# Optimization experiments

Hardware: AMD Instinct MI355X
Metric: run time of the kernel (lower is better)

## Reference

```python
import jax, jax.numpy as jnp
import numpy as np

MAX_FRAMES = 12
EMBED_DIM = 512
TOPK = 12
NUM_SAMPLES = 500
SIGMA = 0.05
SEL_DIM = 2
NUM_HEADS = 2


def setup_inputs() -> dict:
    key = jax.random.key(0)
    ks = jax.random.split(key, 9)
    D = EMBED_DIM
    C = D // 2
    s = lambda fan_in: 1.0 / np.sqrt(fan_in)
    return {
        "x": jax.random.normal(ks[0], (16, MAX_FRAMES * 50, D), dtype=jnp.float32),
        "ln_g": jnp.ones((D,), jnp.float32),
        "ln_b": jnp.zeros((D,), jnp.float32),
        "w_in": jax.random.normal(ks[1], (D, C), jnp.float32) * s(D),
        "wq": jax.random.normal(ks[2], (C, C), jnp.float32) * s(C),
        "wk": jax.random.normal(ks[3], (C, C), jnp.float32) * s(C),
        "wv": jax.random.normal(ks[4], (C, C), jnp.float32) * s(C),
        "wo": jax.random.normal(ks[5], (C, C), jnp.float32) * s(C),
        "w1": jax.random.normal(ks[6], (2 * C, C), jnp.float32) * s(2 * C),
        "w2": jax.random.normal(ks[7], (C, 1), jnp.float32) * s(C),
    }


def layer_norm(x, g, b, eps=1e-5):
    mu = jnp.mean(x, axis=-1, keepdims=True)
    var = jnp.var(x, axis=-1, keepdims=True)
    return (x - mu) * jax.lax.rsqrt(var + eps) * g + b


def mha(x, wq, wk, wv, wo):
    B, N, C = x.shape
    hd = C // NUM_HEADS
    q = (x @ wq).reshape(B, N, NUM_HEADS, hd).transpose(0, 2, 1, 3)
    k = (x @ wk).reshape(B, N, NUM_HEADS, hd).transpose(0, 2, 1, 3)
    v = (x @ wv).reshape(B, N, NUM_HEADS, hd).transpose(0, 2, 1, 3)
    attn = jax.nn.softmax(jnp.einsum('bhnd,bhmd->bhnm', q, k) / np.sqrt(hd), axis=-1)
    out = jnp.einsum('bhnm,bhmd->bhnd', attn, v).transpose(0, 2, 1, 3).reshape(B, N, C)
    return out @ wo


def predictor(x, ln_g, ln_b, w_in, wq, wk, wv, wo, w1, w2):
    h = jax.nn.gelu(layer_norm(x, ln_g, ln_b) @ w_in, approximate=False)
    h = mha(h, wq, wk, wv, wo)
    B, N, C = h.shape
    g = jnp.mean(h, axis=1, keepdims=True)
    h = jnp.concatenate([h, jnp.broadcast_to(g, (B, N, C))], axis=-1)
    h = jax.nn.gelu(h @ w1, approximate=False)
    return jnp.tanh(h @ w2)  # (B, N, 1)


def perturbed_topk(scores):
    # scores: (b, d) -> soft indicators (b, k, d)
    b, d = scores.shape
    noise = jax.random.normal(jax.random.key(1), (b, NUM_SAMPLES, d), dtype=scores.dtype)
    perturbed = scores[:, None, :] + noise * SIGMA
    _, idx = jax.lax.top_k(perturbed, TOPK)            # (b, ns, k)
    idx = jnp.sort(idx, axis=-1)
    onehot = jax.nn.one_hot(idx, d, dtype=scores.dtype)  # (b, ns, k, d)
    return onehot.mean(axis=1)                          # (b, k, d)


def reference(x, ln_g, ln_b, w_in, wq, wk, wv, wo, w1, w2):
    B, L, D = x.shape
    N = L // MAX_FRAMES
    xf = x.reshape(B * MAX_FRAMES, N, D)
    pred = predictor(xf, ln_g, ln_b, w_in, wq, wk, wv, wo, w1, w2)[..., 0]  # (b, N)
    spatial_score = pred[:, SEL_DIM:]                    # (b, N-2)
    ind = perturbed_topk(spatial_score)                  # (b, k, N-2)
    cls_feat = xf[:, :SEL_DIM, :]
    spatial_feat = xf[:, SEL_DIM:, :]
    sel = jnp.einsum('bkl,bld->bkd', ind, spatial_feat)
    out = jnp.concatenate([cls_feat, sel], axis=1)       # (b, 2+k, D)
    return out.reshape(B, -1, D)
```

## Files before the change

### kernel.cpp

```cpp
#include <hip/hip_runtime.h>
#include <stdint.h>

#define B2      192
#define NTOK    50
#define ROWS    9600
#define D_EMB   512
#define C_DIM   256
#define HD      128
#define NSAMP   500
#define TOPKK   12
#define NSPA    48
#define NSAMP_T 96000
#define NOISE_OFF 61953536ull
#define NOISE_BYTES 18432000ull
#define WS_NEED (NOISE_OFF + NOISE_BYTES)

typedef short short8 __attribute__((ext_vector_type(8)));
typedef float f32x4  __attribute__((ext_vector_type(4)));

__device__ __forceinline__ float gelu_f(float x) {
    return 0.5f * x * (1.0f + erff(x * 0.7071067811865476f));
}
__device__ __forceinline__ uint16_t f2bf(float x) {
    uint32_t u = __float_as_uint(x);
    return (uint16_t)((u + 0x7fffu + ((u >> 16) & 1u)) >> 16);
}
__device__ __forceinline__ float bf2f(uint16_t b) {
    return __uint_as_float(((uint32_t)b) << 16);
}
__device__ __forceinline__ size_t swzA(int m, int k, int K) {
    return ((size_t)(m >> 4) * (K >> 5) + (k >> 5)) * 512
         + (size_t)((((k >> 3) & 3) * 16 + (m & 15)) * 8 + (k & 7));
}

__device__ __forceinline__ uint32_t rotl32(uint32_t x, int r) {
    return (x << r) | (x >> (32 - r));
}
__device__ __forceinline__ void threefry01(uint32_t& x0, uint32_t& x1) {
    const uint32_t ks0 = 0u, ks1 = 1u, ks2 = 0x1BD11BDBu;
    x0 += ks0; x1 += ks1;
#define TFR(r) { x0 += x1; x1 = rotl32(x1, r); x1 ^= x0; }
    TFR(13) TFR(15) TFR(26) TFR(6)  x0 += ks1; x1 += ks2 + 1u;
    TFR(17) TFR(29) TFR(16) TFR(24) x0 += ks2; x1 += ks0 + 2u;
    TFR(13) TFR(15) TFR(26) TFR(6)  x0 += ks0; x1 += ks1 + 3u;
    TFR(17) TFR(29) TFR(16) TFR(24) x0 += ks1; x1 += ks2 + 4u;
    TFR(13) TFR(15) TFR(26) TFR(6)  x0 += ks2; x1 += ks0 + 5u;
#undef TFR
}

__device__ __forceinline__ float erfinv_xla(float x) {
    float w = -log1pf(-x * x);
    float p;
    if (w < 5.0f) {
        w -= 2.5f;
        p = 2.81022636e-08f;
        p = fmaf(p, w, 3.43273939e-07f);
        p = fmaf(p, w, -3.5233877e-06f);
        p = fmaf(p, w, -4.39150654e-06f);
        p = fmaf(p, w, 0.00021858087f);
        p = fmaf(p, w, -0.00125372503f);
        p = fmaf(p, w, -0.00417768164f);
        p = fmaf(p, w, 0.246640727f);
        p = fmaf(p, w, 1.50140941f);
    } else {
        w = sqrtf(w) - 3.0f;
        p = -0.000200214257f;
        p = fmaf(p, w, 0.000100950558f);
        p = fmaf(p, w, 0.00134934322f);
        p = fmaf(p, w, -0.00367342844f);
        p = fmaf(p, w, 0.00573950773f);
        p = fmaf(p, w, -0.0076224613f);
        p = fmaf(p, w, 0.00943887047f);
        p = fmaf(p, w, 1.00167406f);
        p = fmaf(p, w, 2.83297682f);
    }
    return p * x;
}

__device__ __forceinline__ float bits_to_normal(uint32_t bits) {
    float f = __uint_as_float((bits >> 9) | 0x3f800000u) - 1.0f;
    float u = f * 2.0f + (-0.99999994039535522461f);
    u = fmaxf(-0.99999994039535522461f, u);
    return 1.4142135623730951f * erfinv_xla(u);
}

__global__ __launch_bounds__(256) void noise_kernel(float* __restrict__ noise) {
    int T  = blockIdx.x * 256 + threadIdx.x;
    int q  = T / NSAMP_T;
    int g2 = T - q * NSAMP_T;
    uint32_t cbase = (uint32_t)g2 * 48u + (uint32_t)(q * 4);
    float4 o;
    { uint32_t x0=0u, x1=cbase + 0u; threefry01(x0,x1); o.x = bits_to_normal(x0^x1) * 0.05f; }
    { uint32_t x0=0u, x1=cbase + 1u; threefry01(x0,x1); o.y = bits_to_normal(x0^x1) * 0.05f; }
    { uint32_t x0=0u, x1=cbase + 2u; threefry01(x0,x1); o.z = bits_to_normal(x0^x1) * 0.05f; }
    { uint32_t x0=0u, x1=cbase + 3u; threefry01(x0,x1); o.w = bits_to_normal(x0^x1) * 0.05f; }
    ((float4*)noise)[(size_t)q * NSAMP_T + g2] = o;
}

__global__ __launch_bounds__(256) void prep_kernel(const float* __restrict__ x,
                                                   const float* __restrict__ g,
                                                   const float* __restrict__ b,
                                                   short* __restrict__ xh,
                                                   short* __restrict__ xl,
                                                   const float* __restrict__ w_in, const float* __restrict__ wq,
                                                   const float* __restrict__ wk, const float* __restrict__ wv,
                                                   const float* __restrict__ wo, const float* __restrict__ w1,
                                                   short* win_hi, short* win_lo, short* wq_hi, short* wq_lo,
                                                   short* wk_hi, short* wk_lo, short* wv_hi, short* wv_lo,
                                                   short* wo_hi, short* wo_lo, short* w1a_hi, short* w1a_lo) {
    if (blockIdx.x < 2400) {
        int row  = blockIdx.x * 4 + (threadIdx.x >> 6);
        int lane = threadIdx.x & 63;
        const float* rp = x + (size_t)row * D_EMB;
        float4 v0 = *(const float4*)(rp + lane * 8);
        float4 v1 = *(const float4*)(rp + lane * 8 + 4);
        float s  = v0.x + v0.y + v0.z + v0.w + v1.x + v1.y + v1.z + v1.w;
        float s2 = v0.x*v0.x + v0.y*v0.y + v0.z*v0.z + v0.w*v0.w
                 + v1.x*v1.x + v1.y*v1.y + v1.z*v1.z + v1.w*v1.w;
#pragma unroll
        for (int off = 32; off; off >>= 1) {
            s  += __shfl_xor(s,  off);
            s2 += __shfl_xor(s2, off);
        }
        float mu  = s / 512.0f;
        float var = s2 / 512.0f - mu * mu;
        float inv = 1.0f / sqrtf(var + 1e-5f);
        const float* gp = g + lane * 8;
        const float* bp = b + lane * 8;
        float o[8];
        o[0]=(v0.x-mu)*inv*gp[0]+bp[0]; o[1]=(v0.y-mu)*inv*gp[1]+bp[1];
        o[2]=(v0.z-mu)*inv*gp[2]+bp[2]; o[3]=(v0.w-mu)*inv*gp[3]+bp[3];
        o[4]=(v1.x-mu)*inv*gp[4]+bp[4]; o[5]=(v1.y-mu)*inv*gp[5]+bp[5];
        o[6]=(v1.z-mu)*inv*gp[6]+bp[6]; o[7]=(v1.w-mu)*inv*gp[7]+bp[7];
        short8 h8, l8;
#pragma unroll
        for (int j = 0; j < 8; ++j) {
            uint16_t h = f2bf(o[j]);
            h8[j] = (short)h;
            l8[j] = (short)f2bf(o[j] - bf2f(h));
        }
        size_t blk = (size_t)(row >> 4) * 16 + (lane >> 2);
        int inner  = (lane & 3) * 16 + (row & 15);
        ((short8*)xh)[blk * 64 + inner] = h8;
        ((short8*)xl)[blk * 64 + inner] = l8;
    } else {
        int blk = blockIdx.x - 2400;
        const float* W; short *hi, *lo; int K, base;
        if      (blk <  64) { W = w_in; hi = win_hi; lo = win_lo; K = 512; base = 0;   }
        else if (blk <  96) { W = wq;   hi = wq_hi;  lo = wq_lo;  K = 256; base = 64;  }
        else if (blk < 128) { W = wk;   hi = wk_hi;  lo = wk_lo;  K = 256; base = 96;  }
        else if (blk < 160) { W = wv;   hi = wv_hi;  lo = wv_lo;  K = 256; base = 128; }
        else if (blk < 192) { W = wo;   hi = wo_hi;  lo = wo_lo;  K = 256; base = 160; }
        else                { W = w1;   hi = w1a_hi; lo = w1a_lo; K = 256; base = 192; }
        int t = (blk - base) * 256 + threadIdx.x;
        int n = t & 255, k8 = t >> 8;
        short8 h8, l8;
#pragma unroll
        for (int j = 0; j < 8; ++j) {
            float wvl = W[(size_t)(k8 * 8 + j) * 256 + n];
            uint16_t h = f2bf(wvl);
            h8[j] = (short)h;
            l8[j] = (short)f2bf(wvl - bf2f(h));
        }
        size_t bb = (size_t)(n >> 4) * (K >> 5) + (k8 >> 2);
        int inner = (k8 & 3) * 16 + (n & 15);
        ((short8*)hi)[bb * 64 + inner] = h8;
        ((short8*)lo)[bb * 64 + inner] = l8;
    }
}

template<int KB>
__device__ __forceinline__ void mm_core(const short8* __restrict__ pAh, const short8* __restrict__ pAl,
                                        const short8* __restrict__ pBh0, const short8* __restrict__ pBl0,
                                        const short8* __restrict__ pBh1, const short8* __restrict__ pBl1,
                                        f32x4& acc0, f32x4& acc1) {
    short8 ah[3], al[3], bh0[3], bl0[3], bh1[3], bl1[3];
#pragma unroll
    for (int i = 0; i < 2; ++i) {
        int off = i * 64;
        ah[i] = pAh[off];  al[i] = pAl[off];
        bh0[i] = pBh0[off]; bl0[i] = pBl0[off];
        bh1[i] = pBh1[off]; bl1[i] = pBl1[off];
    }
#pragma unroll
    for (int ks = 0; ks < KB; ++ks) {
        int cur = ks % 3;
        if (ks + 2 < KB) {
            int pre = (ks + 2) % 3, off = (ks + 2) * 64;
            ah[pre] = pAh[off];  al[pre] = pAl[off];
            bh0[pre] = pBh0[off]; bl0[pre] = pBl0[off];
            bh1[pre] = pBh1[off]; bl1[pre] = pBl1[off];
        }
        acc0 = __builtin_amdgcn_mfma_f32_16x16x32_bf16(ah[cur], bh0[cur], acc0, 0, 0, 0);
        acc0 = __builtin_amdgcn_mfma_f32_16x16x32_bf16(ah[cur], bl0[cur], acc0, 0, 0, 0);
        acc0 = __builtin_amdgcn_mfma_f32_16x16x32_bf16(al[cur], bh0[cur], acc0, 0, 0, 0);
        acc1 = __builtin_amdgcn_mfma_f32_16x16x32_bf16(ah[cur], bh1[cur], acc1, 0, 0, 0);
        acc1 = __builtin_amdgcn_mfma_f32_16x16x32_bf16(ah[cur], bl1[cur], acc1, 0, 0, 0);
        acc1 = __builtin_amdgcn_mfma_f32_16x16x32_bf16(al[cur], bh1[cur], acc1, 0, 0, 0);
    }
}

__device__ __forceinline__ void epi_store(f32x4 acc, int row0, int col, int N,
                                          float* __restrict__ Cf, short* __restrict__ Chi,
                                          short* __restrict__ Clo,
                                          const float* __restrict__ bias, int act) {
#pragma unroll
    for (int r = 0; r < 4; ++r) {
        int row = row0 + r;
        float v2 = acc[r];
        if (bias) v2 += bias[(size_t)(row / 50) * N + col];
        if (act)  v2 = gelu_f(v2);
        if (Cf) Cf[(size_t)row * N + col] = v2;
        if (Chi) {
            uint16_t h = f2bf(v2);
            size_t ad = swzA(row, col, 256);
            Chi[ad] = (short)h;
            Clo[ad] = (short)f2bf(v2 - bf2f(h));
        }
    }
}

template<int KB>
__global__ __launch_bounds__(256) void gemm_one(const short8* __restrict__ Ah,
                                                const short8* __restrict__ Al,
                                                const short8* __restrict__ Bh,
                                                const short8* __restrict__ Bl,
                                                float* __restrict__ Cf,
                                                short* __restrict__ Chi,
                                                short* __restrict__ Clo,
                                                const float* __restrict__ bias,
                                                int act) {
    int lane = threadIdx.x & 63;
    int wv   = threadIdx.x >> 6;
    int ms   = blockIdx.x * 4 + wv;
    int ns0  = blockIdx.y * 2;
    const short8* pAh  = Ah + (size_t)ms  * KB * 64 + lane;
    const short8* pAl  = Al + (size_t)ms  * KB * 64 + lane;
    const short8* pBh0 = Bh + (size_t)ns0 * KB * 64 + lane;
    const short8* pBl0 = Bl + (size_t)ns0 * KB * 64 + lane;
    const short8* pBh1 = pBh0 + (size_t)KB * 64;
    const short8* pBl1 = pBl0 + (size_t)KB * 64;
    f32x4 acc0 = {0.f,0.f,0.f,0.f}, acc1 = {0.f,0.f,0.f,0.f};
    mm_core<KB>(pAh, pAl, pBh0, pBl0, pBh1, pBl1, acc0, acc1);
    int row0 = ms * 16 + (lane >> 4) * 4;
    int cin  = lane & 15;
    epi_store(acc0, row0, ns0 * 16 + cin,      256, Cf, Chi, Clo, bias, act);
    epi_store(acc1, row0, (ns0 + 1) * 16 + cin, 256, Cf, Chi, Clo, bias, act);
}

__global__ __launch_bounds__(256) void gemm8_pred(const short8* __restrict__ Ah,
                                                  const short8* __restrict__ Al,
                                                  const short8* __restrict__ Bh,
                                                  const short8* __restrict__ Bl,
                                                  const float* __restrict__ gwb,
                                                  const float* __restrict__ w2,
                                                  float* __restrict__ pred_raw) {
    int lane = threadIdx.x & 63;
    int wv   = threadIdx.x >> 6;
    int ms   = blockIdx.x * 4 + wv;
    int ns0  = blockIdx.y * 2;
    const short8* pAh  = Ah + (size_t)ms  * 8 * 64 + lane;
    const short8* pAl  = Al + (size_t)ms  * 8 * 64 + lane;
    const short8* pBh0 = Bh + (size_t)ns0 * 8 * 64 + lane;
    const short8* pBl0 = Bl + (size_t)ns0 * 8 * 64 + lane;
    const short8* pBh1 = pBh0 + 8 * 64;
    const short8* pBl1 = pBl0 + 8 * 64;
    f32x4 acc0 = {0.f,0.f,0.f,0.f}, acc1 = {0.f,0.f,0.f,0.f};
    mm_core<8>(pAh, pAl, pBh0, pBl0, pBh1, pBl1, acc0, acc1);
    int row0 = ms * 16 + (lane >> 4) * 4;
    int cin  = lane & 15;
    int c0   = ns0 * 16 + cin;
    int c1   = (ns0 + 1) * 16 + cin;
    float w2a = w2[c0], w2b = w2[c1];
#pragma unroll
    for (int r = 0; r < 4; ++r) {
        int row = row0 + r;
        int bb  = row / 50;
        float v0 = gelu_f(acc0[r] + gwb[(size_t)bb * 256 + c0]);
        float v1 = gelu_f(acc1[r] + gwb[(size_t)bb * 256 + c1]);
        float t  = v0 * w2a + v1 * w2b;
        t += __shfl_xor(t, 1); t += __shfl_xor(t, 2);
        t += __shfl_xor(t, 4); t += __shfl_xor(t, 8);
        if (cin == 0) atomicAdd(&pred_raw[row], t);
    }
}

__global__ __launch_bounds__(256) void gemm_qkv(const short8* __restrict__ Ah,
                                                const short8* __restrict__ Al,
                                                const short8* __restrict__ Bhq, const short8* __restrict__ Blq,
                                                const short8* __restrict__ Bhk, const short8* __restrict__ Blk,
                                                const short8* __restrict__ Bhv, const short8* __restrict__ Blv,
                                                float* __restrict__ q, float* __restrict__ k,
                                                float* __restrict__ v) {
    int lane = threadIdx.x & 63;
    int wv   = threadIdx.x >> 6;
    int ms   = blockIdx.x * 4 + wv;
    int sel  = blockIdx.y >> 3;
    int ns0  = (blockIdx.y & 7) * 2;
    const short8* Bh = (sel == 0) ? Bhq : (sel == 1) ? Bhk : Bhv;
    const short8* Bl = (sel == 0) ? Blq : (sel == 1) ? Blk : Blv;
    float* C = (sel == 0) ? q : (sel == 1) ? k : v;
    const short8* pAh  = Ah + (size_t)ms  * 8 * 64 + lane;
    const short8* pAl  = Al + (size_t)ms  * 8 * 64 + lane;
    const short8* pBh0 = Bh + (size_t)ns0 * 8 * 64 + lane;
    const short8* pBl0 = Bl + (size_t)ns0 * 8 * 64 + lane;
    const short8* pBh1 = pBh0 + 8 * 64;
    const short8* pBl1 = pBl0 + 8 * 64;
    f32x4 acc0 = {0.f,0.f,0.f,0.f}, acc1 = {0.f,0.f,0.f,0.f};
    mm_core<8>(pAh, pAl, pBh0, pBl0, pBh1, pBl1, acc0, acc1);
    int row0 = ms * 16 + (lane >> 4) * 4;
    int cin  = lane & 15;
    epi_store(acc0, row0, ns0 * 16 + cin,      256, C, nullptr, nullptr, nullptr, 0);
    epi_store(acc1, row0, (ns0 + 1) * 16 + cin, 256, C, nullptr, nullptr, nullptr, 0);
}

#define ASLOT(r, s) ((r) * 128 + (((s) ^ (((r) >> 2) & 7)) << 2))
__global__ __launch_bounds__(256) void attn_kernel(const float* __restrict__ q,
                                                   const float* __restrict__ k,
                                                   const float* __restrict__ v,
                                                   short* __restrict__ aoh,
                                                   short* __restrict__ aol) {
    __shared__ float sQ[NTOK * 128];
    __shared__ float sK[NTOK * 128];
    __shared__ float sS[NTOK * 51];
    int blk = blockIdx.x;
    int b = blk >> 1, h = blk & 1;
    const size_t base = (size_t)b * NTOK * C_DIM + h * HD;
    int tid = threadIdx.x;
    for (int idx = tid; idx < 1600; idx += 256) {
        int r = idx >> 5, s = idx & 31;
        int ps = ASLOT(r, s);
        *(float4*)&sQ[ps] = *(const float4*)(q + base + (size_t)r * C_DIM + s * 4);
        *(float4*)&sK[ps] = *(const float4*)(k + base + (size_t)r * C_DIM + s * 4);
    }
    __syncthreads();
    if (tid < 169) {
        int i2 = tid / 13, j2 = tid - i2 * 13;
        int i0 = i2 * 4, j0 = j2 * 4;
        int kq = i2 & 7, kk = j2 & 7;
        const float* qp[4];
        const float* kp[4];
#pragma unroll
        for (int r = 0; r < 4; ++r) {
            int ir = i0 + r; if (ir > 49) ir = 49;
            int jr = j0 + r; if (jr > 49) jr = 49;
            qp[r] = &sQ[ir * 128];
            kp[r] = &sK[jr * 128];
        }
        f32x4 acc[4][4];
#pragma unroll
        for (int r = 0; r < 4; ++r)
#pragma unroll
            for (int c = 0; c < 4; ++c) acc[r][c] = (f32x4){0.f, 0.f, 0.f, 0.f};
#pragma unroll 4
        for (int t = 0; t < 32; ++t) {
            int oq = (t ^ kq) << 2, ok = (t ^ kk) << 2;
            f32x4 qr[4], kr[4];
#pragma unroll
            for (int r = 0; r < 4; ++r) qr[r] = *(const f32x4*)(qp[r] + oq);
#pragma unroll
            for (int c = 0; c < 4; ++c) kr[c] = *(const f32x4*)(kp[c] + ok);
#pragma unroll
            for (int r = 0; r < 4; ++r)
#pragma unroll
                for (int c = 0; c < 4; ++c) acc[r][c] += qr[r] * kr[c];
        }
        const float sc = 0.08838834764831845f;
#pragma unroll
        for (int r = 0; r < 4; ++r) {
            if (i0 + r < 50) {
#pragma unroll
                for (int c = 0; c < 4; ++c) {
                    if (j0 + c < 50) {
                        f32x4 a = acc[r][c];
                        sS[(i0 + r) * 51 + (j0 + c)] = (a[0] + a[1] + a[2] + a[3]) * sc;
                    }
                }
            }
        }
    }
    __syncthreads();
    for (int idx = tid; idx < 1600; idx += 256) {
        int r = idx >> 5, s = idx & 31;
        *(float4*)&sQ[ASLOT(r, s)] = *(const float4*)(v + base + (size_t)r * C_DIM + s * 4);
    }
    {
        int wid = tid >> 6, lane = tid & 63;
        for (int i = wid; i < NTOK; i += 4) {
            float val = (lane < NTOK) ? sS[i * 51 + lane] : -3.0e38f;
            float m = val;
#pragma unroll
            for (int off = 32; off; off >>= 1) m = fmaxf(m, __shfl_xor(m, off));
            float e2 = expf(val - m);
            float s = e2;
#pragma unroll
            for (int off = 32; off; off >>= 1) s += __shfl_xor(s, off);
            if (lane < NTOK) sS[i * 51 + lane] = e2 * (1.0f / s);
        }
    }
    __syncthreads();
    for (int e = tid; e < 416; e += 256) {
        int i2 = e >> 5;
        int s4 = e & 31;
        int i0 = i2 * 4;
        const float* sr[4];
#pragma unroll
        for (int r = 0; r < 4; ++r) {
            int ir = i0 + r; if (ir > 49) ir = 49;
            sr[r] = &sS[ir * 51];
        }
        f32x4 acc[4];
#pragma unroll
        for (int r = 0; r < 4; ++r) acc[r] = (f32x4){0.f, 0.f, 0.f, 0.f};
        for (int j = 0; j < NTOK; ++j) {
            f32x4 v4 = *(const f32x4*)&sQ[ASLOT(j, s4)];
#pragma unroll
            for (int r = 0; r < 4; ++r) acc[r] += v4 * sr[r][j];
        }
#pragma unroll
        for (int r = 0; r < 4; ++r) {
            if (i0 + r < 50) {
                int row = b * NTOK + i0 + r;
#pragma unroll
                for (int c = 0; c < 4; ++c) {
                    int col = h * HD + s4 * 4 + c;
                    float val = acc[r][c];
                    uint16_t hh2 = f2bf(val);
                    size_t ad = swzA(row, col, 256);
                    aoh[ad] = (short)hh2;
                    aol[ad] = (short)f2bf(val - bf2f(hh2));
                }
            }
        }
    }
}
#undef ASLOT

__global__ __launch_bounds__(256) void mean_gw(const float* __restrict__ h2,
                                               const float* __restrict__ w1,
                                               float* __restrict__ gw,
                                               float* __restrict__ pred_raw) {
    __shared__ float sg[C_DIM];
    int b = blockIdx.x, d = threadIdx.x;
    if (d < NTOK) pred_raw[b * NTOK + d] = 0.0f;
    float s = 0.f;
    for (int n = 0; n < NTOK; ++n) s += h2[((size_t)b * NTOK + n) * C_DIM + d];
    sg[d] = s * 0.02f;
    __syncthreads();
    const float* wb = w1 + 256 * 256;
    float acc = 0.f;
#pragma unroll 4
    for (int k = 0; k < C_DIM; ++k)
        acc = fmaf(sg[k], wb[(size_t)k * 256 + d], acc);
    gw[(size_t)b * C_DIM + d] = acc;
}

#define STEP(li) { unsigned long long mn_ = (key < li) ? key : li; \
                   li = (key > li) ? key : li; key = mn_; }
#define S1  STEP(l0)
#define S2  S1  STEP(l1)
#define S3  S2  STEP(l2)
#define S4  S3  STEP(l3)
#define S5  S4  STEP(l4)
#define S6  S5  STEP(l5)
#define S7  S6  STEP(l6)
#define S8  S7  STEP(l7)
#define S9  S8  STEP(l8)
#define S10 S9  STEP(l9)
#define S11 S10 STEP(l10)
#define S12 S11 STEP(l11)

template<int NZ>
__global__ __launch_bounds__(1024, 4) void topk_select(const float* __restrict__ pred,
                                                       const float4* __restrict__ nz4,
                                                       const float* __restrict__ x,
                                                       float* __restrict__ out) {
    __shared__ unsigned long long sK[500][13];
    __shared__ int scnt[TOPKK * NSPA];
    __shared__ float sSP[NSPA];
    __shared__ int anyl[NSPA];
    int b   = blockIdx.x;
    int tid = threadIdx.x;
    int hh  = tid >> 9;
    int s   = tid & 511;
    for (int i = tid; i < TOPKK * NSPA; i += 1024) scnt[i] = 0;
    if (tid < NSPA) sSP[tid] = tanhf(pred[b * NTOK + 2 + tid]);
    __syncthreads();
    bool act = (s < NSAMP);

    unsigned long long l0=0ull,l1=0ull,l2=0ull,l3=0ull,l4=0ull,l5=0ull,
                       l6=0ull,l7=0ull,l8=0ull,l9=0ull,l10=0ull,l11=0ull;
    unsigned long long key;
    if (act) {
        if (NZ) {
            const float* spl = &sSP[hh * 24];
            int g = b * NSAMP + s;
            const float4* nq = nz4 + (size_t)(hh * 6) * NSAMP_T + g;
            float4 n0 = nq[0 * NSAMP_T], n1 = nq[1 * NSAMP_T], n2 = nq[2 * NSAMP_T];
            float4 n3 = nq[3 * NSAMP_T], n4 = nq[4 * NSAMP_T], n5 = nq[5 * NSAMP_T];
#define MKKEY(dd, nv) { float v_ = spl[dd] + (nv); uint32_t vb_ = __float_as_uint(v_); \
    uint32_t mono_ = (vb_ & 0x80000000u) ? ~vb_ : (vb_ | 0x80000000u); \
    key = ((unsigned long long)mono_ << 6) | (unsigned)(63 - (hh * 24 + (dd))); }
            MKKEY(0,  n0.x) S1   MKKEY(1,  n0.y) S2   MKKEY(2,  n0.z) S3   MKKEY(3,  n0.w) S4
            MKKEY(4,  n1.x) S5   MKKEY(5,  n1.y) S6   MKKEY(6,  n1.z) S7   MKKEY(7,  n1.w) S8
            MKKEY(8,  n2.x) S9   MKKEY(9,  n2.y) S10  MKKEY(10, n2.z) S11  MKKEY(11, n2.w) S12
            MKKEY(12, n3.x) S12  MKKEY(13, n3.y) S12  MKKEY(14, n3.z) S12  MKKEY(15, n3.w) S12
            MKKEY(16, n4.x) S12  MKKEY(17, n4.y) S12  MKKEY(18, n4.z) S12  MKKEY(19, n4.w) S12
            MKKEY(20, n5.x) S12  MKKEY(21, n5.y) S12  MKKEY(22, n5.z) S12  MKKEY(23, n5.w) S12
#undef MKKEY
        } else {
            uint32_t base = (uint32_t)((b * NSAMP + s) * NSPA);
            int d0 = hh * 24;
#define FBKEY(dd) { int d_ = d0 + (dd); uint32_t x0_ = 0u, x1_ = base + (uint32_t)d_; \
    threefry01(x0_, x1_); float v_ = sSP[d_] + bits_to_normal(x0_ ^ x1_) * 0.05f; \
    uint32_t vb_ = __float_as_uint(v_); \
    uint32_t mono_ = (vb_ & 0x80000000u) ? ~vb_ : (vb_ | 0x80000000u); \
    key = ((unsigned long long)mono_ << 6) | (unsigned)(63 - d_); }
            FBKEY(0)  S1   FBKEY(1)  S2   FBKEY(2)  S3   FBKEY(3)  S4
            FBKEY(4)  S5   FBKEY(5)  S6   FBKEY(6)  S7   FBKEY(7)  S8
            FBKEY(8)  S9   FBKEY(9)  S10  FBKEY(10) S11  FBKEY(11) S12
#pragma unroll 2
            for (int dd = 12; dd < 24; ++dd) { FBKEY(dd) S12 }
#undef FBKEY
        }
        if (hh == 1) {
            unsigned long long* r = sK[s];
            r[0]=l0; r[1]=l1; r[2]=l2;  r[3]=l3;  r[4]=l4;   r[5]=l5;
            r[6]=l6; r[7]=l7; r[8]=l8;  r[9]=l9;  r[10]=l10; r[11]=l11;
        }
    }
    __syncthreads();
    if (act && hh == 0) {
        const unsigned long long* r = sK[s];
        unsigned long long M0  = (l0  > r[11]) ? l0  : r[11];
        unsigned long long M1  = (l1  > r[10]) ? l1  : r[10];
        unsigned long long M2  = (l2  > r[9])  ? l2  : r[9];
        unsigned long long M3  = (l3  > r[8])  ? l3  : r[8];
        unsigned long long M4  = (l4  > r[7])  ? l4  : r[7];
        unsigned long long M5  = (l5  > r[6])  ? l5  : r[6];
        unsigned long long M6  = (l6  > r[5])  ? l6  : r[5];
        unsigned long long M7  = (l7  > r[4])  ? l7  : r[4];
        unsigned long long M8  = (l8  > r[3])  ? l8  : r[3];
        unsigned long long M9  = (l9  > r[2])  ? l9  : r[2];
        unsigned long long M10 = (l10 > r[1])  ? l10 : r[1];
        unsigned long long M11 = (l11 > r[0])  ? l11 : r[0];
        unsigned long long m = 0ull;
        m |= 1ull << (unsigned)(M0  & 63ull);  m |= 1ull << (unsigned)(M1  & 63ull);
        m |= 1ull << (unsigned)(M2  & 63ull);  m |= 1ull << (unsigned)(M3  & 63ull);
        m |= 1ull << (unsigned)(M4  & 63ull);  m |= 1ull << (unsigned)(M5  & 63ull);
        m |= 1ull << (unsigned)(M6  & 63ull);  m |= 1ull << (unsigned)(M7  & 63ull);
        m |= 1ull << (unsigned)(M8  & 63ull);  m |= 1ull << (unsigned)(M9  & 63ull);
        m |= 1ull << (unsigned)(M10 & 63ull);  m |= 1ull << (unsigned)(M11 & 63ull);
#define EMIT(Mi) { unsigned a_ = (unsigned)(Mi & 63ull); \
                   int kpos_ = 11 - __popcll(m & ((1ull << a_) - 1ull)); \
                   int d_ = 63 - (int)a_; \
                   atomicAdd(&scnt[kpos_ * NSPA + d_], 1); }
        EMIT(M0)  EMIT(M1)  EMIT(M2)  EMIT(M3)  EMIT(M4)  EMIT(M5)
        EMIT(M6)  EMIT(M7)  EMIT(M8)  EMIT(M9)  EMIT(M10) EMIT(M11)
#undef EMIT
    }
    __syncthreads();
    if (tid < NSPA) {
        int a = 0;
#pragma unroll
        for (int k2 = 0; k2 < TOPKK; ++k2) a |= scnt[k2 * NSPA + tid];
        anyl[tid] = a;
    }
    __syncthreads();
    if (hh == 0) {
        const float* xr0 = x + (size_t)(b * NTOK) * D_EMB;
        out[(size_t)(b * 14 + 0) * D_EMB + s] = xr0[s];
        out[(size_t)(b * 14 + 1) * D_EMB + s] = xr0[D_EMB + s];
    }
    float a0, a1, a2, a3, a4, a5;
    a0 = a1 = a2 = a3 = a4 = a5 = 0.f;
    int k0 = hh * 6;
    for (int l = 0; l < NSPA; ++l) {
        if (!anyl[l]) continue;
        float v = x[((size_t)(b * NTOK + 2 + l)) * D_EMB + s];
        a0 = fmaf((float)scnt[(k0 + 0) * NSPA + l] * 0.002f, v, a0);
        a1 = fmaf((float)scnt[(k0 + 1) * NSPA + l] * 0.002f, v, a1);
        a2 = fmaf((float)scnt[(k0 + 2) * NSPA + l] * 0.002f, v, a2);
        a3 = fmaf((float)scnt[(k0 + 3) * NSPA + l] * 0.002f, v, a3);
        a4 = fmaf((float)scnt[(k0 + 4) * NSPA + l] * 0.002f, v, a4);
        a5 = fmaf((float)scnt[(k0 + 5) * NSPA + l] * 0.002f, v, a5);
    }
    out[(size_t)(b * 14 + 2 + k0 + 0) * D_EMB + s] = a0;
    out[(size_t)(b * 14 + 2 + k0 + 1) * D_EMB + s] = a1;
    out[(size_t)(b * 14 + 2 + k0 + 2) * D_EMB + s] = a2;
    out[(size_t)(b * 14 + 2 + k0 + 3) * D_EMB + s] = a3;
    out[(size_t)(b * 14 + 2 + k0 + 4) * D_EMB + s] = a4;
    out[(size_t)(b * 14 + 2 + k0 + 5) * D_EMB + s] = a5;
}
#undef STEP
#undef S1
#undef S2
#undef S3
#undef S4
#undef S5
#undef S6
#undef S7
#undef S8
#undef S9
#undef S10
#undef S11
#undef S12

extern "C" void kernel_launch(void* const* d_in, const int* in_sizes, int n_in,
                              void* d_out, int out_size, void* d_ws, size_t ws_size,
                              hipStream_t stream) {
    const float* x    = (const float*)d_in[0];
    const float* ln_g = (const float*)d_in[1];
    const float* ln_b = (const float*)d_in[2];
    const float* w_in = (const float*)d_in[3];
    const float* wq   = (const float*)d_in[4];
    const float* wk   = (const float*)d_in[5];
    const float* wv   = (const float*)d_in[6];
    const float* wo   = (const float*)d_in[7];
    const float* w1   = (const float*)d_in[8];
    const float* w2   = (const float*)d_in[9];
    float* out = (float*)d_out;

    char* W = (char*)d_ws;
    short* xn_hi  = (short*)(W + 0);
    short* xn_lo  = (short*)(W + 9830400);
    short* ao_hi  = (short*)(W + 0);
    short* ao_lo  = (short*)(W + 4915200);
    short* h2_hi  = (short*)(W + 9830400);
    short* h2_lo  = (short*)(W + 14745600);
    short* h1_hi  = (short*)(W + 19660800);
    short* h1_lo  = (short*)(W + 24576000);
    float* q      = (float*)(W + 29491200);
    float* h2f    = (float*)(W + 29491200);
    float* k      = (float*)(W + 39321600);
    float* v      = (float*)(W + 49152000);
    short* win_hi = (short*)(W + 58982400);
    short* win_lo = (short*)(W + 59244544);
    short* wq_hi  = (short*)(W + 59506688);
    short* wq_lo  = (short*)(W + 59637760);
    short* wk_hi  = (short*)(W + 59768832);
    short* wk_lo  = (short*)(W + 59899904);
    short* wv_hi  = (short*)(W + 60030976);
    short* wv_lo  = (short*)(W + 60162048);
    short* wo_hi  = (short*)(W + 60293120);
    short* wo_lo  = (short*)(W + 60424192);
    short* w1a_hi = (short*)(W + 60555264);
    short* w1a_lo = (short*)(W + 60686336);
    float* gw     = (float*)(W + 61276160);
    float* pred   = (float*)(W + 61472768);
    float* noise  = (float*)(W + NOISE_OFF);

    const bool nzmode = ws_size >= WS_NEED;

    if (nzmode) noise_kernel<<<4500, 256, 0, stream>>>(noise);
    prep_kernel<<<2624, 256, 0, stream>>>(x, ln_g, ln_b, xn_hi, xn_lo,
        w_in, wq, wk, wv, wo, w1,
        win_hi, win_lo, wq_hi, wq_lo, wk_hi, wk_lo, wv_hi, wv_lo,
        wo_hi, wo_lo, w1a_hi, w1a_lo);
    gemm_one<16><<<dim3(150, 8), 256, 0, stream>>>((const short8*)xn_hi, (const short8*)xn_lo,
        (const short8*)win_hi, (const short8*)win_lo, nullptr, h1_hi, h1_lo, nullptr, 1);
    gemm_qkv<<<dim3(150, 24), 256, 0, stream>>>((const short8*)h1_hi, (const short8*)h1_lo,
        (const short8*)wq_hi, (const short8*)wq_lo, (const short8*)wk_hi, (const short8*)wk_lo,
        (const short8*)wv_hi, (const short8*)wv_lo, q, k, v);
    attn_kernel<<<B2 * 2, 256, 0, stream>>>(q, k, v, ao_hi, ao_lo);
    gemm_one<8><<<dim3(150, 8), 256, 0, stream>>>((const short8*)ao_hi, (const short8*)ao_lo,
        (const short8*)wo_hi, (const short8*)wo_lo, h2f, h2_hi, h2_lo, nullptr, 0);
    mean_gw<<<B2, 256, 0, stream>>>(h2f, w1, gw, pred);
    gemm8_pred<<<dim3(150, 8), 256, 0, stream>>>((const short8*)h2_hi, (const short8*)h2_lo,
        (const short8*)w1a_hi, (const short8*)w1a_lo, gw, w2, pred);
    if (nzmode) topk_select<1><<<B2, 1024, 0, stream>>>(pred, (const float4*)noise, x, out);
    else        topk_select<0><<<B2, 1024, 0, stream>>>(pred, nullptr, x, out);
}
```

Before: 275.5 us.

## Fold noise generation into first GEMM and mean/gw into prediction GEMM

Noise generation now runs in extra blocks of the first GEMM launch instead of its own kernel, so the RNG work can overlap the matmul. The separate mean_gw kernel is removed. Each gemm8_pred block recomputes the token mean and its slice of the global-feature projection in shared memory, and the pred buffer is zeroed inside the wo GEMM. This cuts two launches and their serialization, at the cost of redundant mean/projection work repeated across the 8 column blocks for the same batch rows.

```diff
diff --git a/kernel.cpp b/kernel.cpp
--- a/kernel.cpp
+++ b/kernel.cpp
@@ -84,19 +84,6 @@
     return 1.4142135623730951f * erfinv_xla(u);
 }
 
-__global__ __launch_bounds__(256) void noise_kernel(float* __restrict__ noise) {
-    int T  = blockIdx.x * 256 + threadIdx.x;
-    int q  = T / NSAMP_T;
-    int g2 = T - q * NSAMP_T;
-    uint32_t cbase = (uint32_t)g2 * 48u + (uint32_t)(q * 4);
-    float4 o;
-    { uint32_t x0=0u, x1=cbase + 0u; threefry01(x0,x1); o.x = bits_to_normal(x0^x1) * 0.05f; }
-    { uint32_t x0=0u, x1=cbase + 1u; threefry01(x0,x1); o.y = bits_to_normal(x0^x1) * 0.05f; }
-    { uint32_t x0=0u, x1=cbase + 2u; threefry01(x0,x1); o.z = bits_to_normal(x0^x1) * 0.05f; }
-    { uint32_t x0=0u, x1=cbase + 3u; threefry01(x0,x1); o.w = bits_to_normal(x0^x1) * 0.05f; }
-    ((float4*)noise)[(size_t)q * NSAMP_T + g2] = o;
-}
-
 __global__ __launch_bounds__(256) void prep_kernel(const float* __restrict__ x,
                                                    const float* __restrict__ g,
                                                    const float* __restrict__ b,
@@ -202,13 +189,11 @@
 
 __device__ __forceinline__ void epi_store(f32x4 acc, int row0, int col, int N,
                                           float* __restrict__ Cf, short* __restrict__ Chi,
-                                          short* __restrict__ Clo,
-                                          const float* __restrict__ bias, int act) {
+                                          short* __restrict__ Clo, int act) {
 #pragma unroll
     for (int r = 0; r < 4; ++r) {
         int row = row0 + r;
         float v2 = acc[r];
-        if (bias) v2 += bias[(size_t)(row / 50) * N + col];
         if (act)  v2 = gelu_f(v2);
         if (Cf) Cf[(size_t)row * N + col] = v2;
         if (Chi) {
@@ -220,69 +205,45 @@
     }
 }
 
-template<int KB>
-__global__ __launch_bounds__(256) void gemm_one(const short8* __restrict__ Ah,
-                                                const short8* __restrict__ Al,
-                                                const short8* __restrict__ Bh,
-                                                const short8* __restrict__ Bl,
-                                                float* __restrict__ Cf,
-                                                short* __restrict__ Chi,
-                                                short* __restrict__ Clo,
-                                                const float* __restrict__ bias,
-                                                int act) {
+__global__ __launch_bounds__(256) void gemm16_nz(const short8* __restrict__ Ah,
+                                                 const short8* __restrict__ Al,
+                                                 const short8* __restrict__ Bh,
+                                                 const short8* __restrict__ Bl,
+                                                 short* __restrict__ Chi,
+                                                 short* __restrict__ Clo,
+                                                 float* __restrict__ noise) {
+    if (blockIdx.x >= 150) {
+        int nb = (blockIdx.x - 150) * 8 + blockIdx.y;
+        if (nb < 4500) {
+            int T  = nb * 256 + threadIdx.x;
+            int q  = T / NSAMP_T;
+            int g2 = T - q * NSAMP_T;
+            uint32_t cbase = (uint32_t)g2 * 48u + (uint32_t)(q * 4);
+            float4 o;
+            { uint32_t x0=0u, x1=cbase + 0u; threefry01(x0,x1); o.x = bits_to_normal(x0^x1) * 0.05f; }
+            { uint32_t x0=0u, x1=cbase + 1u; threefry01(x0,x1); o.y = bits_to_normal(x0^x1) * 0.05f; }
+            { uint32_t x0=0u, x1=cbase + 2u; threefry01(x0,x1); o.z = bits_to_normal(x0^x1) * 0.05f; }
+            { uint32_t x0=0u, x1=cbase + 3u; threefry01(x0,x1); o.w = bits_to_normal(x0^x1) * 0.05f; }
+            ((float4*)noise)[(size_t)q * NSAMP_T + g2] = o;
+        }
+        return;
+    }
     int lane = threadIdx.x & 63;
     int wv   = threadIdx.x >> 6;
     int ms   = blockIdx.x * 4 + wv;
     int ns0  = blockIdx.y * 2;
-    const short8* pAh  = Ah + (size_t)ms  * KB * 64 + lane;
-    const short8* pAl  = Al + (size_t)ms  * KB * 64 + lane;
-    const short8* pBh0 = Bh + (size_t)ns0 * KB * 64 + lane;
-    const short8* pBl0 = Bl + (size_t)ns0 * KB * 64 + lane;
-    const short8* pBh1 = pBh0 + (size_t)KB * 64;
-    const short8* pBl1 = pBl0 + (size_t)KB * 64;
+    const short8* pAh  = Ah + (size_t)ms  * 16 * 64 + lane;
+    const short8* pAl  = Al + (size_t)ms  * 16 * 64 + lane;
+    const short8* pBh0 = Bh + (size_t)ns0 * 16 * 64 + lane;
+    const short8* pBl0 = Bl + (size_t)ns0 * 16 * 64 + lane;
+    const short8* pBh1 = pBh0 + (size_t)16 * 64;
+    const short8* pBl1 = pBl0 + (size_t)16 * 64;
     f32x4 acc0 = {0.f,0.f,0.f,0.f}, acc1 = {0.f,0.f,0.f,0.f};
-    mm_core<KB>(pAh, pAl, pBh0, pBl0, pBh1, pBl1, acc0, acc1);
+    mm_core<16>(pAh, pAl, pBh0, pBl0, pBh1, pBl1, acc0, acc1);
     int row0 = ms * 16 + (lane >> 4) * 4;
     int cin  = lane & 15;
-    epi_store(acc0, row0, ns0 * 16 + cin,      256, Cf, Chi, Clo, bias, act);
-    epi_store(acc1, row0, (ns0 + 1) * 16 + cin, 256, Cf, Chi, Clo, bias, act);
-}
-
-__global__ __launch_bounds__(256) void gemm8_pred(const short8* __restrict__ Ah,
-                                                  const short8* __restrict__ Al,
-                                                  const short8* __restrict__ Bh,
-                                                  const short8* __restrict__ Bl,
-                                                  const float* __restrict__ gwb,
-                                                  const float* __restrict__ w2,
-                                                  float* __restrict__ pred_raw) {
-    int lane = threadIdx.x & 63;
-    int wv   = threadIdx.x >> 6;
-    int ms   = blockIdx.x * 4 + wv;
-    int ns0  = blockIdx.y * 2;
-    const short8* pAh  = Ah + (size_t)ms  * 8 * 64 + lane;
-    const short8* pAl  = Al + (size_t)ms  * 8 * 64 + lane;
-    const short8* pBh0 = Bh + (size_t)ns0 * 8 * 64 + lane;
-    const short8* pBl0 = Bl + (size_t)ns0 * 8 * 64 + lane;
-    const short8* pBh1 = pBh0 + 8 * 64;
-    const short8* pBl1 = pBl0 + 8 * 64;
-    f32x4 acc0 = {0.f,0.f,0.f,0.f}, acc1 = {0.f,0.f,0.f,0.f};
-    mm_core<8>(pAh, pAl, pBh0, pBl0, pBh1, pBl1, acc0, acc1);
-    int row0 = ms * 16 + (lane >> 4) * 4;
-    int cin  = lane & 15;
-    int c0   = ns0 * 16 + cin;
-    int c1   = (ns0 + 1) * 16 + cin;
-    float w2a = w2[c0], w2b = w2[c1];
-#pragma unroll
-    for (int r = 0; r < 4; ++r) {
-        int row = row0 + r;
-        int bb  = row / 50;
-        float v0 = gelu_f(acc0[r] + gwb[(size_t)bb * 256 + c0]);
-        float v1 = gelu_f(acc1[r] + gwb[(size_t)bb * 256 + c1]);
-        float t  = v0 * w2a + v1 * w2b;
-        t += __shfl_xor(t, 1); t += __shfl_xor(t, 2);
-        t += __shfl_xor(t, 4); t += __shfl_xor(t, 8);
-        if (cin == 0) atomicAdd(&pred_raw[row], t);
-    }
+    epi_store(acc0, row0, ns0 * 16 + cin,      256, nullptr, Chi, Clo, 1);
+    epi_store(acc1, row0, (ns0 + 1) * 16 + cin, 256, nullptr, Chi, Clo, 1);
 }
 
 __global__ __launch_bounds__(256) void gemm_qkv(const short8* __restrict__ Ah,
@@ -310,8 +271,8 @@
     mm_core<8>(pAh, pAl, pBh0, pBl0, pBh1, pBl1, acc0, acc1);
     int row0 = ms * 16 + (lane >> 4) * 4;
     int cin  = lane & 15;
-    epi_store(acc0, row0, ns0 * 16 + cin,      256, C, nullptr, nullptr, nullptr, 0);
-    epi_store(acc1, row0, (ns0 + 1) * 16 + cin, 256, C, nullptr, nullptr, nullptr, 0);
+    epi_store(acc0, row0, ns0 * 16 + cin,      256, C, nullptr, nullptr, 0);
+    epi_store(acc1, row0, (ns0 + 1) * 16 + cin, 256, C, nullptr, nullptr, 0);
 }
 
 #define ASLOT(r, s) ((r) * 128 + (((s) ^ (((r) >> 2) & 7)) << 2))
@@ -436,23 +397,92 @@
 }
 #undef ASLOT
 
-__global__ __launch_bounds__(256) void mean_gw(const float* __restrict__ h2,
-                                               const float* __restrict__ w1,
-                                               float* __restrict__ gw,
-                                               float* __restrict__ pred_raw) {
-    __shared__ float sg[C_DIM];
-    int b = blockIdx.x, d = threadIdx.x;
-    if (d < NTOK) pred_raw[b * NTOK + d] = 0.0f;
-    float s = 0.f;
-    for (int n = 0; n < NTOK; ++n) s += h2[((size_t)b * NTOK + n) * C_DIM + d];
-    sg[d] = s * 0.02f;
-    __syncthreads();
-    const float* wb = w1 + 256 * 256;
-    float acc = 0.f;
+__global__ __launch_bounds__(256) void gemm8_wo(const short8* __restrict__ Ah,
+                                                const short8* __restrict__ Al,
+                                                const short8* __restrict__ Bh,
+                                                const short8* __restrict__ Bl,
+                                                float* __restrict__ Cf,
+                                                short* __restrict__ Chi,
+                                                short* __restrict__ Clo,
+                                                float* __restrict__ pred_raw) {
+    if (blockIdx.y == 0 && threadIdx.x < 64)
+        pred_raw[blockIdx.x * 64 + threadIdx.x] = 0.0f;
+    int lane = threadIdx.x & 63;
+    int wv   = threadIdx.x >> 6;
+    int ms   = blockIdx.x * 4 + wv;
+    int ns0  = blockIdx.y * 2;
+    const short8* pAh  = Ah + (size_t)ms  * 8 * 64 + lane;
+    const short8* pAl  = Al + (size_t)ms  * 8 * 64 + lane;
+    const short8* pBh0 = Bh + (size_t)ns0 * 8 * 64 + lane;
+    const short8* pBl0 = Bl + (size_t)ns0 * 8 * 64 + lane;
+    const short8* pBh1 = pBh0 + 8 * 64;
+    const short8* pBl1 = pBl0 + 8 * 64;
+    f32x4 acc0 = {0.f,0.f,0.f,0.f}, acc1 = {0.f,0.f,0.f,0.f};
+    mm_core<8>(pAh, pAl, pBh0, pBl0, pBh1, pBl1, acc0, acc1);
+    int row0 = ms * 16 + (lane >> 4) * 4;
+    int cin  = lane & 15;
+    epi_store(acc0, row0, ns0 * 16 + cin,      256, Cf, Chi, Clo, 0);
+    epi_store(acc1, row0, (ns0 + 1) * 16 + cin, 256, Cf, Chi, Clo, 0);
+}
+
+__global__ __launch_bounds__(256) void gemm8_pred(const short8* __restrict__ Ah,
+                                                  const short8* __restrict__ Al,
+                                                  const short8* __restrict__ Bh,
+                                                  const short8* __restrict__ Bl,
+                                                  const float* __restrict__ h2f,
+                                                  const float* __restrict__ w1,
+                                                  const float* __restrict__ w2,
+                                                  float* __restrict__ pred_raw) {
+    __shared__ float sgm[3][C_DIM];
+    __shared__ float sgw[3][32];
+    int xb = blockIdx.x, yb = blockIdx.y;
+    int d  = threadIdx.x;
+    int b0 = (xb * 64) / 50;
+    int nb = ((xb * 64 + 63) / 50) - b0 + 1;
+    for (int bi = 0; bi < nb; ++bi) {
+        const float* hp = h2f + (size_t)(b0 + bi) * 50 * C_DIM + d;
+        float s = 0.f;
+        for (int n = 0; n < NTOK; ++n) s += hp[(size_t)n * C_DIM];
+        sgm[bi][d] = s * 0.02f;
+    }
+    __syncthreads();
+    if (d < nb * 32) {
+        int bi = d >> 5, cc = d & 31;
+        const float* wb = w1 + 256 * 256 + yb * 32 + cc;
+        float acc = 0.f;
 #pragma unroll 4
-    for (int k = 0; k < C_DIM; ++k)
-        acc = fmaf(sg[k], wb[(size_t)k * 256 + d], acc);
-    gw[(size_t)b * C_DIM + d] = acc;
+        for (int k2 = 0; k2 < C_DIM; ++k2) acc = fmaf(sgm[bi][k2], wb[(size_t)k2 * 256], acc);
+        sgw[bi][cc] = acc;
+    }
+    __syncthreads();
+    int lane = threadIdx.x & 63;
+    int wv   = threadIdx.x >> 6;
+    int ms   = xb * 4 + wv;
+    int ns0  = yb * 2;
+    const short8* pAh  = Ah + (size_t)ms  * 8 * 64 + lane;
+    const short8* pAl  = Al + (size_t)ms  * 8 * 64 + lane;
+    const short8* pBh0 = Bh + (size_t)ns0 * 8 * 64 + lane;
+    const short8* pBl0 = Bl + (size_t)ns0 * 8 * 64 + lane;
+    const short8* pBh1 = pBh0 + 8 * 64;
+    const short8* pBl1 = pBl0 + 8 * 64;
+    f32x4 acc0 = {0.f,0.f,0.f,0.f}, acc1 = {0.f,0.f,0.f,0.f};
+    mm_core<8>(pAh, pAl, pBh0, pBl0, pBh1, pBl1, acc0, acc1);
+    int row0 = ms * 16 + (lane >> 4) * 4;
+    int cin  = lane & 15;
+    int c0   = ns0 * 16 + cin;
+    int c1   = (ns0 + 1) * 16 + cin;
+    float w2a = w2[c0], w2b = w2[c1];
+#pragma unroll
+    for (int r = 0; r < 4; ++r) {
+        int row = row0 + r;
+        int bi  = row / 50 - b0;
+        float v0 = gelu_f(acc0[r] + sgw[bi][cin]);
+        float v1 = gelu_f(acc1[r] + sgw[bi][16 + cin]);
+        float t  = v0 * w2a + v1 * w2b;
+        t += __shfl_xor(t, 1); t += __shfl_xor(t, 2);
+        t += __shfl_xor(t, 4); t += __shfl_xor(t, 8);
+        if (cin == 0) atomicAdd(&pred_raw[row], t);
+    }
 }
 
 #define STEP(li) { unsigned long long mn_ = (key < li) ? key : li; \
@@ -646,28 +676,26 @@
     short* wo_lo  = (short*)(W + 60424192);
     short* w1a_hi = (short*)(W + 60555264);
     short* w1a_lo = (short*)(W + 60686336);
-    float* gw     = (float*)(W + 61276160);
     float* pred   = (float*)(W + 61472768);
     float* noise  = (float*)(W + NOISE_OFF);
 
     const bool nzmode = ws_size >= WS_NEED;
 
-    if (nzmode) noise_kernel<<<4500, 256, 0, stream>>>(noise);
     prep_kernel<<<2624, 256, 0, stream>>>(x, ln_g, ln_b, xn_hi, xn_lo,
         w_in, wq, wk, wv, wo, w1,
         win_hi, win_lo, wq_hi, wq_lo, wk_hi, wk_lo, wv_hi, wv_lo,
         wo_hi, wo_lo, w1a_hi, w1a_lo);
-    gemm_one<16><<<dim3(150, 8), 256, 0, stream>>>((const short8*)xn_hi, (const short8*)xn_lo,
-        (const short8*)win_hi, (const short8*)win_lo, nullptr, h1_hi, h1_lo, nullptr, 1);
+    gemm16_nz<<<dim3(nzmode ? 713 : 150, 8), 256, 0, stream>>>(
+        (const short8*)xn_hi, (const short8*)xn_lo,
+        (const short8*)win_hi, (const short8*)win_lo, h1_hi, h1_lo, noise);
     gemm_qkv<<<dim3(150, 24), 256, 0, stream>>>((const short8*)h1_hi, (const short8*)h1_lo,
         (const short8*)wq_hi, (const short8*)wq_lo, (const short8*)wk_hi, (const short8*)wk_lo,
         (const short8*)wv_hi, (const short8*)wv_lo, q, k, v);
     attn_kernel<<<B2 * 2, 256, 0, stream>>>(q, k, v, ao_hi, ao_lo);
-    gemm_one<8><<<dim3(150, 8), 256, 0, stream>>>((const short8*)ao_hi, (const short8*)ao_lo,
-        (const short8*)wo_hi, (const short8*)wo_lo, h2f, h2_hi, h2_lo, nullptr, 0);
-    mean_gw<<<B2, 256, 0, stream>>>(h2f, w1, gw, pred);
+    gemm8_wo<<<dim3(150, 8), 256, 0, stream>>>((const short8*)ao_hi, (const short8*)ao_lo,
+        (const short8*)wo_hi, (const short8*)wo_lo, h2f, h2_hi, h2_lo, pred);
     gemm8_pred<<<dim3(150, 8), 256, 0, stream>>>((const short8*)h2_hi, (const short8*)h2_lo,
-        (const short8*)w1a_hi, (const short8*)w1a_lo, gw, w2, pred);
+        (const short8*)w1a_hi, (const short8*)w1a_lo, h2f, w1, w2, pred);
     if (nzmode) topk_select<1><<<B2, 1024, 0, stream>>>(pred, (const float4*)noise, x, out);
     else        topk_select<0><<<B2, 1024, 0, stream>>>(pred, nullptr, x, out);
 }
```

After: 264.1 us. 4.1% less time.
